# Optimization experiments

Hardware: AMD Instinct MI355X
Metric: run time of the kernel (lower is better)

The kernel has to match this reference:

```python
import jax, jax.numpy as jnp
import numpy as np

NQ = 4          # n_qubits -> 2**4 = 16 amplitudes
NL = 3          # n_layers
TWO_PI = 2.0 * np.pi
BN_EPS = 1e-5


def _ry_batched(t):
    # t: [B] -> [B,2,2] complex64
    c, s = jnp.cos(t / 2), jnp.sin(t / 2)
    g = jnp.stack([jnp.stack([c, -s], -1), jnp.stack([s, c], -1)], -2)
    return g.astype(jnp.complex64)


def _ry(t):
    c, s = jnp.cos(t / 2), jnp.sin(t / 2)
    return jnp.stack([jnp.stack([c, -s]), jnp.stack([s, c])]).astype(jnp.complex64)


def _rz(t):
    e = jnp.stack([jnp.exp(-0.5j * t), jnp.exp(0.5j * t)]).astype(jnp.complex64)
    return jnp.diag(e)


def _apply_1q(state, gate, wire, batched):
    # state: [B,2,2,2,2]; gate: [2,2] or [B,2,2]
    s = jnp.moveaxis(state, wire + 1, -1)
    if batched:
        s = jnp.einsum('bij,b...j->b...i', gate, s)
    else:
        s = jnp.einsum('ij,...j->...i', gate, s)
    return jnp.moveaxis(s, -1, wire + 1)


def _apply_cnot(state, c, t):
    s = jnp.moveaxis(state, (c + 1, t + 1), (-2, -1))
    s = jnp.stack([s[..., 0, :], s[..., 1, ::-1]], axis=-2)  # flip target when control=1
    return jnp.moveaxis(s, (-2, -1), (c + 1, t + 1))


def _circuit(angles, weights):
    # angles: [B, NQ] float32; weights: [NL, NQ, 2]
    B = angles.shape[0]
    state = jnp.zeros((B,) + (2,) * NQ, jnp.complex64)
    state = state.at[(slice(None),) + (0,) * NQ].set(1.0)
    # input encoding RYs (per-sample angles -> batched gates)
    for i in range(NQ):
        state = _apply_1q(state, _ry_batched(angles[:, i]), i, True)
    for layer in range(NL):
        for i in range(NQ):
            state = _apply_1q(state, _ry(weights[layer, i, 0]), i, False)
            state = _apply_1q(state, _rz(weights[layer, i, 1]), i, False)
        for i in range(NQ - 1):
            state = _apply_cnot(state, i, i + 1)
        state = _apply_cnot(state, NQ - 1, 0)
    probs = jnp.abs(state) ** 2  # [B,2,2,2,2] real
    zs = []
    for i in range(NQ):
        axes = tuple(a for a in range(1, NQ + 1) if a != i + 1)
        pm = probs.sum(axis=axes)  # [B,2]
        zs.append(pm[:, 0] - pm[:, 1])
    return jnp.stack(zs, -1).astype(jnp.float32)  # [B,NQ]


def setup_inputs() -> dict:
    key = jax.random.key(0)
    ks = jax.random.split(key, 4)
    B = 524288
    x = jax.random.normal(ks[0], (B, 16), jnp.float32)
    weights = jax.random.normal(ks[1], (NL, NQ, 2), jnp.float32)
    fc_w = jax.random.normal(ks[2], (4, NQ), jnp.float32) / np.sqrt(NQ)
    fc_b = jax.random.normal(ks[3], (4,), jnp.float32) * 0.01
    gamma = jnp.ones((4,), jnp.float32)
    beta = jnp.zeros((4,), jnp.float32)
    return {"x": x, "weights": weights, "fc_w": fc_w, "fc_b": fc_b,
            "gamma": gamma, "beta": beta}


def reference(x, weights, fc_w, fc_b, gamma, beta):
    inp = x.reshape(x.shape[0], -1)[:, :NQ]
    mn, mx = inp.min(), inp.max()  # global min/max as in the torch code
    angles = TWO_PI * (inp - mn) / (mx - mn + 1e-8)
    q = _circuit(angles, weights)                # [B,4] PauliZ expvals
    out = q @ fc_w.T + fc_b                      # Linear(4,4)
    mean = out.mean(0)
    var = out.var(0)                             # biased, as torch BN training
    return gamma * (out - mean) / jnp.sqrt(var + BN_EPS) + beta
```

## Files before the change

kernel.cpp:

```cpp
#include <hip/hip_runtime.h>
#include <math.h>

#define TWO_PI_F 6.28318530717958647692f
#define BN_EPS_F 1e-5f

#define NBLK 1024
#define NT 256
#define NLEAF 32
#define MKSH 16
#define STSH 8

#define NB1 2048
#define NB2 1024

#define MK_OFF 0
#define LEAFA_OFF 512
#define FLAGA_OFF 1536
#define ROOTA_OFF 2560
#define LEAFB_OFF 2592
#define FLAGB_OFF 3616
#define ROOTB_OFF 4640
#define UZERO_N 5696
#define STAT_OFF 4672
#define CTAB_OFF 5696
#define BMIN_OFF 256
#define BMAX_OFF 2304
#define TAB_OFF 4352
#define SSLOT_OFF 4992

__device__ __forceinline__ unsigned fkey(float f) {
  unsigned u = __float_as_uint(f);
  return u ^ (unsigned(int(u) >> 31) | 0x80000000u);
}
__device__ __forceinline__ float funkey(unsigned k) {
  unsigned u = (k & 0x80000000u) ? (k ^ 0x80000000u) : ~k;
  return __uint_as_float(u);
}

__device__ __forceinline__ void build_ucol(int col, const float* __restrict__ w,
                                           float* sr, float* si) {
#pragma unroll
  for (int k = 0; k < 16; ++k) { sr[k] = (k == col) ? 1.f : 0.f; si[k] = 0.f; }
#pragma unroll
  for (int l = 0; l < 3; ++l) {
#pragma unroll
    for (int i = 0; i < 4; ++i) {
      const int m = 8 >> i;
      float ryc, rys, rzc, rzs;
      __sincosf(0.5f * w[(l * 4 + i) * 2 + 0], &rys, &ryc);
      __sincosf(0.5f * w[(l * 4 + i) * 2 + 1], &rzs, &rzc);
#pragma unroll
      for (int k = 0; k < 16; ++k) {
        if (!(k & m)) {
          int k1 = k | m;
          float a0r = sr[k], a0i = si[k], a1r = sr[k1], a1i = si[k1];
          sr[k] = ryc * a0r - rys * a1r;
          si[k] = ryc * a0i - rys * a1i;
          sr[k1] = rys * a0r + ryc * a1r;
          si[k1] = rys * a0i + ryc * a1i;
        }
      }
#pragma unroll
      for (int k = 0; k < 16; ++k) {
        float ps = (k & m) ? rzs : -rzs;
        float rr = sr[k], ii = si[k];
        sr[k] = rr * rzc - ii * ps;
        si[k] = rr * ps + ii * rzc;
      }
    }
#pragma unroll
    for (int c = 0; c < 4; ++c) {
      const int mc = 8 >> c;
      const int mt = 8 >> ((c + 1) & 3);
#pragma unroll
      for (int k = 0; k < 16; ++k) {
        if ((k & mc) && !(k & mt)) {
          int k2 = k | mt;
          float tt;
          tt = sr[k]; sr[k] = sr[k2]; sr[k2] = tt;
          tt = si[k]; si[k] = si[k2]; si[k2] = tt;
        }
      }
    }
  }
}

__global__ __launch_bounds__(128) void k0_init(const float* __restrict__ w,
                                               const float* __restrict__ fc_w,
                                               float* __restrict__ wsf) {
  int tid = threadIdx.x;
  unsigned* u = (unsigned*)wsf;
  for (int i = tid; i < UZERO_N; i += 128) u[i] = 0u;
  __syncthreads();
  if (tid < 16) {
    float sr[16], si[16];
    build_ucol(tid, w, sr, si);
#pragma unroll
    for (int k = 0; k < 16; ++k) {
      wsf[CTAB_OFF + tid * 16 + k] = sr[k];
      wsf[CTAB_OFF + 256 + tid * 16 + k] = si[k];
    }
  } else if (tid < 32) {
    u[MK_OFF + (tid - 16) * 32] = 0xFFFFFFFFu;
  } else if (tid >= 64 && tid < 128) {
    int e = tid - 64, k = e >> 2, j = e & 3;
    float s = 0.f;
#pragma unroll
    for (int i = 0; i < 4; ++i)
      s += fc_w[j * 4 + i] * ((k & (8 >> i)) ? -1.f : 1.f);
    wsf[CTAB_OFF + 512 + k * 4 + j] = s;
  }
}

__device__ __forceinline__ void grid_barrier(unsigned* __restrict__ leaf,
                                             unsigned* __restrict__ flag,
                                             unsigned* __restrict__ root) {
  __syncthreads();
  if (threadIdx.x == 0) {
    const int l = (int)(blockIdx.x >> 5);
    unsigned p = __hip_atomic_fetch_add(leaf + l * 32, 1u, __ATOMIC_RELAXED,
                                        __HIP_MEMORY_SCOPE_AGENT);
    if (p == 31u) {
      unsigned q = __hip_atomic_fetch_add(root, 1u, __ATOMIC_RELAXED,
                                          __HIP_MEMORY_SCOPE_AGENT);
      if (q == (unsigned)(NLEAF - 1)) {
#pragma unroll
        for (int f = 0; f < NLEAF; ++f)
          __hip_atomic_store(flag + f * 32, 1u, __ATOMIC_RELAXED,
                             __HIP_MEMORY_SCOPE_AGENT);
      }
    }
    while (__hip_atomic_load(flag + l * 32, __ATOMIC_RELAXED,
                             __HIP_MEMORY_SCOPE_AGENT) == 0u)
      __builtin_amdgcn_s_sleep(16);
    asm volatile("" ::: "memory");
  }
  __syncthreads();
}

__device__ __forceinline__ void qfc_one(const float* __restrict__ tab,
                                        const float* c, const float* s,
                                        float* o) {
  const float* __restrict__ Ur = tab;
  const float* __restrict__ Ui = tab + 256;
  const float* __restrict__ At = tab + 512;
  float A01[4] = {c[0] * c[1], c[0] * s[1], s[0] * c[1], s[0] * s[1]};
  float A23[4] = {c[2] * c[3], c[2] * s[3], s[2] * c[3], s[2] * s[3]};
  float yr[16], yi[16];
#pragma unroll
  for (int k = 0; k < 16; ++k) { yr[k] = yi[k] = 0.f; }
#pragma unroll
  for (int a = 0; a < 16; ++a) {
    float va = A01[a >> 2] * A23[a & 3];
#pragma unroll
    for (int k = 0; k < 16; ++k) {
      yr[k] = fmaf(Ur[a * 16 + k], va, yr[k]);
      yi[k] = fmaf(Ui[a * 16 + k], va, yi[k]);
    }
  }
#pragma unroll
  for (int j = 0; j < 4; ++j) o[j] = 0.f;
#pragma unroll
  for (int k = 0; k < 16; ++k) {
    float p = fmaf(yr[k], yr[k], yi[k] * yi[k]);
#pragma unroll
    for (int j = 0; j < 4; ++j) o[j] = fmaf(At[k * 4 + j], p, o[j]);
  }
}

__global__ __launch_bounds__(NT, 4) void fused(
    const float* __restrict__ x, float* __restrict__ wsf,
    const float* __restrict__ gamma, const float* __restrict__ beta,
    float* __restrict__ out, int B) {
  const int tid = threadIdx.x;
  const int gtid = blockIdx.x * NT + tid;
  const int H = NBLK * NT;
  const int wv = tid >> 6, ln = tid & 63;
  unsigned* __restrict__ u = (unsigned*)wsf;
  const float* __restrict__ tab = wsf + CTAB_OFF;
  float* __restrict__ stat = wsf + STAT_OFF;
  __shared__ float smn[4], smx[4];
  __shared__ float red[4][8];
  __shared__ float sbc[2];
  __shared__ float sst[8];

  const int s0 = gtid, s1 = gtid + H;
  const bool h0 = s0 < B, h1 = s1 < B;
  float4 xa = h0 ? *(const float4*)(x + (size_t)s0 * 16) : make_float4(0, 0, 0, 0);
  float4 xb = h1 ? *(const float4*)(x + (size_t)s1 * 16) : make_float4(0, 0, 0, 0);

  float fmn = __builtin_inff(), fmx = -__builtin_inff();
  if (h0) {
    fmn = fminf(fminf(xa.x, xa.y), fminf(xa.z, xa.w));
    fmx = fmaxf(fmaxf(xa.x, xa.y), fmaxf(xa.z, xa.w));
  }
  if (h1) {
    fmn = fminf(fmn, fminf(fminf(xb.x, xb.y), fminf(xb.z, xb.w)));
    fmx = fmaxf(fmx, fmaxf(fmaxf(xb.x, xb.y), fmaxf(xb.z, xb.w)));
  }
#pragma unroll
  for (int d = 32; d; d >>= 1) {
    fmn = fminf(fmn, __shfl_down(fmn, d));
    fmx = fmaxf(fmx, __shfl_down(fmx, d));
  }
  if (ln == 0) { smn[wv] = fmn; smx[wv] = fmx; }
  __syncthreads();
  if (tid == 0) {
    float bm = fminf(fminf(smn[0], smn[1]), fminf(smn[2], smn[3]));
    float bM = fmaxf(fmaxf(smx[0], smx[1]), fmaxf(smx[2], smx[3]));
    const int sh = (int)(blockIdx.x & (MKSH - 1));
    atomicMin(u + MK_OFF + sh * 32, fkey(bm));
    atomicMax(u + MK_OFF + sh * 32 + 16, fkey(bM));
  }

  grid_barrier(u + LEAFA_OFF, u + FLAGA_OFF, u + ROOTA_OFF);

  if (tid < 32) {
    unsigned k;
    if (tid < 16)
      k = __hip_atomic_load(u + MK_OFF + tid * 32, __ATOMIC_RELAXED,
                            __HIP_MEMORY_SCOPE_AGENT);
    else
      k = __hip_atomic_load(u + MK_OFF + (tid - 16) * 32 + 16, __ATOMIC_RELAXED,
                            __HIP_MEMORY_SCOPE_AGENT);
#pragma unroll
    for (int d = 8; d; d >>= 1) {
      unsigned p = __shfl_xor(k, d);
      k = (tid < 16) ? ((p < k) ? p : k) : ((p > k) ? p : k);
    }
    if (tid == 0) sbc[0] = funkey(k);
    if (tid == 16) sbc[1] = funkey(k);
  }
  __syncthreads();
  const float gm = sbc[0], gM = sbc[1];
  const float ssc = TWO_PI_F * 0.5f / (gM - gm + 1e-8f);

  float a0[4] = {xa.x, xa.y, xa.z, xa.w};
  float a1[4] = {xb.x, xb.y, xb.z, xb.w};
  float c0[4], sn0[4], c1[4], sn1[4];
#pragma unroll
  for (int i = 0; i < 4; ++i) {
    __sincosf((a0[i] - gm) * ssc, &sn0[i], &c0[i]);
    __sincosf((a1[i] - gm) * ssc, &sn1[i], &c1[i]);
  }
  float o0[4], o1[4];
  qfc_one(tab, c0, sn0, o0);
  qfc_one(tab, c1, sn1, o1);

  float vals[8];
#pragma unroll
  for (int j = 0; j < 4; ++j) {
    float v0 = h0 ? o0[j] : 0.f, v1 = h1 ? o1[j] : 0.f;
    vals[j] = v0 + v1;
    vals[4 + j] = fmaf(v0, v0, v1 * v1);
  }
#pragma unroll
  for (int j = 0; j < 8; ++j) {
#pragma unroll
    for (int d = 32; d; d >>= 1) vals[j] += __shfl_down(vals[j], d);
  }
  if (ln == 0) {
#pragma unroll
    for (int j = 0; j < 8; ++j) red[wv][j] = vals[j];
  }
  __syncthreads();
  if (tid < 8) {
    const int sh = (int)(blockIdx.x & (STSH - 1));
    atomicAdd(stat + sh * 16 + tid,
              red[0][tid] + red[1][tid] + red[2][tid] + red[3][tid]);
  }

  grid_barrier(u + LEAFB_OFF, u + FLAGB_OFF, u + ROOTB_OFF);

  if (tid < 64) {
    int s = tid >> 3, j = tid & 7;
    float v = __hip_atomic_load(stat + s * 16 + j, __ATOMIC_RELAXED,
                                __HIP_MEMORY_SCOPE_AGENT);
    v += __shfl_down(v, 32);
    v += __shfl_down(v, 16);
    v += __shfl_down(v, 8);
    if (tid < 8) sst[tid] = v;
  }
  __syncthreads();

  const float inv = 1.0f / (float)B;
  float sc[4], sh[4];
#pragma unroll
  for (int j = 0; j < 4; ++j) {
    float mean = sst[j] * inv;
    float var = sst[4 + j] * inv - mean * mean;
    float is = rsqrtf(var + BN_EPS_F);
    sc[j] = gamma[j] * is;
    sh[j] = beta[j] - mean * sc[j];
  }
  if (h0)
    *(float4*)(out + (size_t)s0 * 4) =
        make_float4(fmaf(o0[0], sc[0], sh[0]), fmaf(o0[1], sc[1], sh[1]),
                    fmaf(o0[2], sc[2], sh[2]), fmaf(o0[3], sc[3], sh[3]));
  if (h1)
    *(float4*)(out + (size_t)s1 * 4) =
        make_float4(fmaf(o1[0], sc[0], sh[0]), fmaf(o1[1], sc[1], sh[1]),
                    fmaf(o1[2], sc[2], sh[2]), fmaf(o1[3], sc[3], sh[3]));
}

__global__ __launch_bounds__(NT) void k1_scan_tab(const float* __restrict__ x,
                                                  const float* __restrict__ w,
                                                  const float* __restrict__ fc_w,
                                                  float* __restrict__ wsf, int B) {
  int r = blockIdx.x * NT + threadIdx.x;
  float fmn = __builtin_inff(), fmx = -__builtin_inff();
  if (r < B) {
    float4 v = *(const float4*)(x + (size_t)r * 16);
    fmn = fminf(fminf(v.x, v.y), fminf(v.z, v.w));
    fmx = fmaxf(fmaxf(v.x, v.y), fmaxf(v.z, v.w));
  }
#pragma unroll
  for (int d = 32; d; d >>= 1) {
    fmn = fminf(fmn, __shfl_down(fmn, d));
    fmx = fmaxf(fmx, __shfl_down(fmx, d));
  }
  __shared__ float smn[4], smx[4];
  int wv = threadIdx.x >> 6, ln = threadIdx.x & 63;
  if (ln == 0) { smn[wv] = fmn; smx[wv] = fmx; }
  __syncthreads();
  if (threadIdx.x == 0) {
    wsf[BMIN_OFF + blockIdx.x] =
        fminf(fminf(smn[0], smn[1]), fminf(smn[2], smn[3]));
    wsf[BMAX_OFF + blockIdx.x] =
        fmaxf(fmaxf(smx[0], smx[1]), fmaxf(smx[2], smx[3]));
  }
  if (blockIdx.x == 0) {
    int tid = threadIdx.x;
    if (tid < 16) {
      float sr[16], si[16];
      build_ucol(tid, w, sr, si);
#pragma unroll
      for (int k = 0; k < 16; ++k) {
        wsf[TAB_OFF + tid * 16 + k] = sr[k];
        wsf[TAB_OFF + 256 + tid * 16 + k] = si[k];
      }
    } else if (tid == 16) {
      for (int k = 0; k < 16; ++k)
        for (int j = 0; j < 4; ++j) {
          float s = 0.f;
          for (int i = 0; i < 4; ++i)
            s += fc_w[j * 4 + i] * ((k & (8 >> i)) ? -1.f : 1.f);
          wsf[TAB_OFF + 512 + k * 4 + j] = s;
        }
    }
  }
}

__device__ __forceinline__ void qfc_pair(const float* __restrict__ tab,
                                         const float* c0, const float* s0,
                                         const float* c1, const float* s1,
                                         float* o0, float* o1) {
  const float* __restrict__ Ur = tab;
  const float* __restrict__ Ui = tab + 256;
  const float* __restrict__ At = tab + 512;
  float A01_0[4] = {c0[0] * c0[1], c0[0] * s0[1], s0[0] * c0[1], s0[0] * s0[1]};
  float A23_0[4] = {c0[2] * c0[3], c0[2] * s0[3], s0[2] * c0[3], s0[2] * s0[3]};
  float A01_1[4] = {c1[0] * c1[1], c1[0] * s1[1], s1[0] * c1[1], s1[0] * s1[1]};
  float A23_1[4] = {c1[2] * c1[3], c1[2] * s1[3], s1[2] * c1[3], s1[2] * s1[3]};
  float yr0[16], yi0[16], yr1[16], yi1[16];
#pragma unroll
  for (int k = 0; k < 16; ++k) { yr0[k] = yi0[k] = yr1[k] = yi1[k] = 0.f; }
#pragma unroll
  for (int a = 0; a < 16; ++a) {
    float va0 = A01_0[a >> 2] * A23_0[a & 3];
    float va1 = A01_1[a >> 2] * A23_1[a & 3];
#pragma unroll
    for (int k = 0; k < 16; ++k) {
      float ur = Ur[a * 16 + k], ui = Ui[a * 16 + k];
      yr0[k] = fmaf(ur, va0, yr0[k]);
      yi0[k] = fmaf(ui, va0, yi0[k]);
      yr1[k] = fmaf(ur, va1, yr1[k]);
      yi1[k] = fmaf(ui, va1, yi1[k]);
    }
  }
#pragma unroll
  for (int j = 0; j < 4; ++j) { o0[j] = 0.f; o1[j] = 0.f; }
#pragma unroll
  for (int k = 0; k < 16; ++k) {
    float p0 = fmaf(yr0[k], yr0[k], yi0[k] * yi0[k]);
    float p1 = fmaf(yr1[k], yr1[k], yi1[k] * yi1[k]);
#pragma unroll
    for (int j = 0; j < 4; ++j) {
      float av = At[k * 4 + j];
      o0[j] = fmaf(av, p0, o0[j]);
      o1[j] = fmaf(av, p1, o1[j]);
    }
  }
}

__global__ __launch_bounds__(NT) void k2_main(const float* __restrict__ x,
                                              const float* __restrict__ wsf,
                                              float* __restrict__ sslot,
                                              float* __restrict__ out, int B) {
  const int tid = threadIdx.x;
  const int gtid = blockIdx.x * NT + tid;
  const int H = NB2 * NT;
  const int wv = tid >> 6, ln = tid & 63;
  const float* __restrict__ tab = wsf + TAB_OFF;

  float gm = __builtin_inff(), gM = -__builtin_inff();
#pragma unroll
  for (int q = 0; q < NB1 / 64; ++q) {
    int i = ln + q * 64;
    gm = fminf(gm, wsf[BMIN_OFF + i]);
    gM = fmaxf(gM, wsf[BMAX_OFF + i]);
  }
#pragma unroll
  for (int d = 32; d; d >>= 1) {
    gm = fminf(gm, __shfl_down(gm, d));
    gM = fmaxf(gM, __shfl_down(gM, d));
  }
  gm = __shfl(gm, 0);
  gM = __shfl(gM, 0);
  const float ssc = TWO_PI_F * 0.5f / (gM - gm + 1e-8f);

  const int s0 = gtid, s1 = gtid + H;
  const bool h0 = s0 < B, h1 = s1 < B;
  float4 xa = h0 ? *(const float4*)(x + (size_t)s0 * 16) : make_float4(0, 0, 0, 0);
  float4 xb = h1 ? *(const float4*)(x + (size_t)s1 * 16) : make_float4(0, 0, 0, 0);

  float a0[4] = {xa.x, xa.y, xa.z, xa.w};
  float a1[4] = {xb.x, xb.y, xb.z, xb.w};
  float c0[4], sn0[4], c1[4], sn1[4];
#pragma unroll
  for (int i = 0; i < 4; ++i) {
    __sincosf((a0[i] - gm) * ssc, &sn0[i], &c0[i]);
    __sincosf((a1[i] - gm) * ssc, &sn1[i], &c1[i]);
  }
  float o0[4], o1[4];
  qfc_pair(tab, c0, sn0, c1, sn1, o0, o1);

  if (h0)
    *(float4*)(out + (size_t)s0 * 4) = make_float4(o0[0], o0[1], o0[2], o0[3]);
  if (h1)
    *(float4*)(out + (size_t)s1 * 4) = make_float4(o1[0], o1[1], o1[2], o1[3]);

  float vals[8];
#pragma unroll
  for (int j = 0; j < 4; ++j) {
    float v0 = h0 ? o0[j] : 0.f, v1 = h1 ? o1[j] : 0.f;
    vals[j] = v0 + v1;
    vals[4 + j] = fmaf(v0, v0, v1 * v1);
  }
#pragma unroll
  for (int j = 0; j < 8; ++j) {
#pragma unroll
    for (int d = 32; d; d >>= 1) vals[j] += __shfl_down(vals[j], d);
  }
  __shared__ float red[4][8];
  if (ln == 0) {
#pragma unroll
    for (int j = 0; j < 8; ++j) red[wv][j] = vals[j];
  }
  __syncthreads();
  if (tid < 8) {
    sslot[blockIdx.x * 8 + tid] =
        red[0][tid] + red[1][tid] + red[2][tid] + red[3][tid];
  }
}

__global__ __launch_bounds__(NT) void k3_final(float* __restrict__ out,
                                               const float* __restrict__ sslot,
                                               const float* __restrict__ gamma,
                                               const float* __restrict__ beta,
                                               int B) {
  const int tid = threadIdx.x;
  const int gtid = blockIdx.x * NT + tid;
  const int H = NB2 * NT;
  const int ln = tid & 63;

  float v = 0.f;
#pragma unroll
  for (int k = 0; k < (NB2 * 8) / 64; ++k) v += sslot[k * 64 + ln];
#pragma unroll
  for (int d = 32; d >= 8; d >>= 1) v += __shfl_down(v, d);
  float st[8];
#pragma unroll
  for (int j = 0; j < 8; ++j) st[j] = __shfl(v, j);

  const float inv = 1.0f / (float)B;
  float sc[4], sh[4];
#pragma unroll
  for (int j = 0; j < 4; ++j) {
    float mean = st[j] * inv;
    float var = st[4 + j] * inv - mean * mean;
    float is = rsqrtf(var + BN_EPS_F);
    sc[j] = gamma[j] * is;
    sh[j] = beta[j] - mean * sc[j];
  }
#pragma unroll
  for (int p = 0; p < 2; ++p) {
    int s = gtid + p * H;
    if (s < B) {
      float4 q = *(float4*)(out + (size_t)s * 4);
      *(float4*)(out + (size_t)s * 4) =
          make_float4(fmaf(q.x, sc[0], sh[0]), fmaf(q.y, sc[1], sh[1]),
                      fmaf(q.z, sc[2], sh[2]), fmaf(q.w, sc[3], sh[3]));
    }
  }
}

extern "C" void kernel_launch(void* const* d_in, const int* in_sizes, int n_in,
                              void* d_out, int out_size, void* d_ws, size_t ws_size,
                              hipStream_t stream) {
  const float* x = (const float*)d_in[0];
  const float* w = (const float*)d_in[1];
  const float* fc_w = (const float*)d_in[2];
  const float* gamma = (const float*)d_in[4];
  const float* beta = (const float*)d_in[5];
  float* out = (float*)d_out;
  float* wsf = (float*)d_ws;
  int B = in_sizes[0] / 16;

  k0_init<<<1, 128, 0, stream>>>(w, fc_w, wsf);

  static int coop_state = -1;
  if (coop_state < 0) {
    int dev = 0;
    (void)hipGetDevice(&dev);
    int ncu = 0;
    (void)hipDeviceGetAttribute(&ncu, hipDeviceAttributeMultiprocessorCount, dev);
    int per_cu = 0;
    (void)hipOccupancyMaxActiveBlocksPerMultiprocessor(&per_cu,
                                                       (const void*)fused, NT, 0);
    coop_state =
        (ncu > 0 && per_cu > 0 && (long long)per_cu * ncu >= NBLK) ? 1 : 0;
  }

  if (coop_state == 1 && B <= 2 * NBLK * NT) {
    fused<<<NBLK, NT, 0, stream>>>(x, wsf, gamma, beta, out, B);
  } else {
    k1_scan_tab<<<NB1, NT, 0, stream>>>(x, w, fc_w, wsf, B);
    k2_main<<<NB2, NT, 0, stream>>>(x, wsf, wsf + SSLOT_OFF, out, B);
    k3_final<<<NB2, NT, 0, stream>>>(out, wsf + SSLOT_OFF, gamma, beta, B);
  }
}
```

Baseline: 118.1 us.

## Replace second grid barrier with separate batchnorm normalization kernel

The fused kernel no longer waits at a second software grid barrier for the batch statistics. It now writes the unnormalized linear outputs to the output buffer and accumulates the statistics. A new small kernel then reads the statistics and rescales the outputs in place. This removes the cost of a grid-wide barrier spin but adds a kernel launch and an extra read and write pass over the 8 MB output.

```diff
diff --git a/kernel.cpp b/kernel.cpp
--- a/kernel.cpp
+++ b/kernel.cpp
@@ -17,9 +17,6 @@
 #define LEAFA_OFF 512
 #define FLAGA_OFF 1536
 #define ROOTA_OFF 2560
-#define LEAFB_OFF 2592
-#define FLAGB_OFF 3616
-#define ROOTB_OFF 4640
 #define UZERO_N 5696
 #define STAT_OFF 4672
 #define CTAB_OFF 5696
@@ -168,9 +165,8 @@
   }
 }
 
-__global__ __launch_bounds__(NT, 4) void fused(
+__global__ __launch_bounds__(NT, 4) void fused2(
     const float* __restrict__ x, float* __restrict__ wsf,
-    const float* __restrict__ gamma, const float* __restrict__ beta,
     float* __restrict__ out, int B) {
   const int tid = threadIdx.x;
   const int gtid = blockIdx.x * NT + tid;
@@ -182,7 +178,6 @@
   __shared__ float smn[4], smx[4];
   __shared__ float red[4][8];
   __shared__ float sbc[2];
-  __shared__ float sst[8];
 
   const int s0 = gtid, s1 = gtid + H;
   const bool h0 = s0 < B, h1 = s1 < B;
@@ -247,6 +242,11 @@
   qfc_one(tab, c0, sn0, o0);
   qfc_one(tab, c1, sn1, o1);
 
+  if (h0)
+    *(float4*)(out + (size_t)s0 * 4) = make_float4(o0[0], o0[1], o0[2], o0[3]);
+  if (h1)
+    *(float4*)(out + (size_t)s1 * 4) = make_float4(o1[0], o1[1], o1[2], o1[3]);
+
   float vals[8];
 #pragma unroll
   for (int j = 0; j < 4; ++j) {
@@ -269,13 +269,22 @@
     atomicAdd(stat + sh * 16 + tid,
               red[0][tid] + red[1][tid] + red[2][tid] + red[3][tid]);
   }
-
-  grid_barrier(u + LEAFB_OFF, u + FLAGB_OFF, u + ROOTB_OFF);
+}
+
+__global__ __launch_bounds__(NT) void k3s(float* __restrict__ out,
+                                          const float* __restrict__ wsf,
+                                          const float* __restrict__ gamma,
+                                          const float* __restrict__ beta,
+                                          int B) {
+  const int tid = threadIdx.x;
+  const int gtid = blockIdx.x * NT + tid;
+  const int H = NB2 * NT;
+  const float* __restrict__ stat = wsf + STAT_OFF;
+  __shared__ float sst[8];
 
   if (tid < 64) {
     int s = tid >> 3, j = tid & 7;
-    float v = __hip_atomic_load(stat + s * 16 + j, __ATOMIC_RELAXED,
-                                __HIP_MEMORY_SCOPE_AGENT);
+    float v = stat[s * 16 + j];
     v += __shfl_down(v, 32);
     v += __shfl_down(v, 16);
     v += __shfl_down(v, 8);
@@ -293,14 +302,16 @@
     sc[j] = gamma[j] * is;
     sh[j] = beta[j] - mean * sc[j];
   }
-  if (h0)
-    *(float4*)(out + (size_t)s0 * 4) =
-        make_float4(fmaf(o0[0], sc[0], sh[0]), fmaf(o0[1], sc[1], sh[1]),
-                    fmaf(o0[2], sc[2], sh[2]), fmaf(o0[3], sc[3], sh[3]));
-  if (h1)
-    *(float4*)(out + (size_t)s1 * 4) =
-        make_float4(fmaf(o1[0], sc[0], sh[0]), fmaf(o1[1], sc[1], sh[1]),
-                    fmaf(o1[2], sc[2], sh[2]), fmaf(o1[3], sc[3], sh[3]));
+#pragma unroll
+  for (int p = 0; p < 2; ++p) {
+    int s = gtid + p * H;
+    if (s < B) {
+      float4 q = *(float4*)(out + (size_t)s * 4);
+      *(float4*)(out + (size_t)s * 4) =
+          make_float4(fmaf(q.x, sc[0], sh[0]), fmaf(q.y, sc[1], sh[1]),
+                      fmaf(q.z, sc[2], sh[2]), fmaf(q.w, sc[3], sh[3]));
+    }
+  }
 }
 
 __global__ __launch_bounds__(NT) void k1_scan_tab(const float* __restrict__ x,
@@ -527,13 +538,14 @@
     (void)hipDeviceGetAttribute(&ncu, hipDeviceAttributeMultiprocessorCount, dev);
     int per_cu = 0;
     (void)hipOccupancyMaxActiveBlocksPerMultiprocessor(&per_cu,
-                                                       (const void*)fused, NT, 0);
+                                                       (const void*)fused2, NT, 0);
     coop_state =
         (ncu > 0 && per_cu > 0 && (long long)per_cu * ncu >= NBLK) ? 1 : 0;
   }
 
   if (coop_state == 1 && B <= 2 * NBLK * NT) {
-    fused<<<NBLK, NT, 0, stream>>>(x, wsf, gamma, beta, out, B);
+    fused2<<<NBLK, NT, 0, stream>>>(x, wsf, out, B);
+    k3s<<<NB2, NT, 0, stream>>>(out, wsf, gamma, beta, B);
   } else {
     k1_scan_tab<<<NB1, NT, 0, stream>>>(x, w, fc_w, wsf, B);
     k2_main<<<NB2, NT, 0, stream>>>(x, wsf, wsf + SSLOT_OFF, out, B);
```

Result: no change. 117.3 us (-0.7%).
